# Optimization experiments

Hardware: AMD Instinct MI355X
Metric: run time of the kernel (lower is better)

Reference implementation:

```python
import jax, jax.numpy as jnp
from jax import lax
import numpy as np

I, H = 2048, 128
EPS = 1e-5


def setup_inputs() -> dict:
    key = jax.random.key(0)
    ks = jax.random.split(key, 12)
    s_ih = 1.0 / np.sqrt(H)  # torch nn.RNN init: U(-1/sqrt(H), 1/sqrt(H))
    s_fc = 1.0 / np.sqrt(H)
    u = lambda k, shape, s: jax.random.uniform(k, shape, jnp.float32, -s, s)
    return {
        "x": jax.random.normal(ks[0], (64, 512, I), jnp.float32),
        "W_ih": u(ks[1], (H, I), s_ih),
        "b_ih": u(ks[2], (H,), s_ih),
        "W_hh": u(ks[3], (H, H), s_ih),
        "b_hh": u(ks[4], (H,), s_ih),
        "W1": u(ks[5], (H, H), s_fc),
        "b1": u(ks[6], (H,), s_fc),
        "W2": u(ks[7], (H, H), s_fc),
        "b2": u(ks[8], (H,), s_fc),
        "gamma": jnp.ones((H,), jnp.float32),
        "beta": jnp.zeros((H,), jnp.float32),
    }


def reference(x, W_ih, b_ih, W_hh, b_hh, W1, b1, W2, b2, gamma, beta):
    B = x.shape[0]
    # Precompute input projection for all timesteps: [B, T, H]
    xp = jnp.einsum('bti,hi->bth', x, W_ih) + b_ih

    def step(h, xt):  # h: [B, H], xt: [B, H]
        h_new = jnp.tanh(xt + h @ W_hh.T + b_hh)
        return h_new, None

    h0 = jnp.zeros((B, H), x.dtype)
    hT, _ = lax.scan(step, h0, jnp.swapaxes(xp, 0, 1))  # scan over T

    z = jax.nn.relu(hT @ W1.T + b1)
    z = jax.nn.relu(z @ W2.T + b2)
    mu = jnp.mean(z, axis=-1, keepdims=True)
    var = jnp.mean(jnp.square(z - mu), axis=-1, keepdims=True)
    return gamma * (z - mu) * lax.rsqrt(var + EPS) + beta
```

## Files before the change

### kernel.cpp

```cpp
#include <hip/hip_runtime.h>


typedef __bf16 bf16x8 __attribute__((ext_vector_type(8)));
typedef float  f32x4  __attribute__((ext_vector_type(4)));

#define T_STEPS 512
#define I_DIM   2048
#define H_DIM   128
#define B_DIM   64
#define M_TOT   (B_DIM * T_STEPS)

__device__ __forceinline__ unsigned short f2bf(float f) {
    unsigned int u = __float_as_uint(f);
    u += 0x7FFFu + ((u >> 16) & 1u);
    return (unsigned short)(u >> 16);
}

#define BM  128
#define BK  64
#define LDK 72

__global__ __launch_bounds__(256) void gemm_xp(
    const float* __restrict__ x,
    const float* __restrict__ w,
    const float* __restrict__ b_ih,
    const float* __restrict__ b_hh,
    float* __restrict__ xp)
{
    __shared__ __align__(16) unsigned short As[BM * LDK];
    __shared__ __align__(16) unsigned short Bs[H_DIM * LDK];

    const int tid = threadIdx.x;
    const int m0  = blockIdx.x * BM;

    const int r0 = tid >> 4;
    const int c4 = tid & 15;

    const int lane = tid & 63;
    const int wave = tid >> 6;
    const int wm   = (wave >> 1) * 64;
    const int wn   = (wave & 1) * 64;
    const int l16  = lane & 15;
    const int quad = lane >> 4;

    f32x4 acc[4][4] = {};

    float4 ar[8], br[8];

    auto load_tiles = [&](int k0) {
        #pragma unroll
        for (int i = 0; i < 8; ++i)
            ar[i] = *(const float4*)(x + (size_t)(m0 + i * 16 + r0) * I_DIM + k0 + c4 * 4);
        #pragma unroll
        for (int i = 0; i < 8; ++i)
            br[i] = *(const float4*)(w + (size_t)(i * 16 + r0) * I_DIM + k0 + c4 * 4);
    };

    auto store_tiles = [&]() {
        #pragma unroll
        for (int i = 0; i < 8; ++i) {
            ushort4 v;
            v.x = f2bf(ar[i].x); v.y = f2bf(ar[i].y);
            v.z = f2bf(ar[i].z); v.w = f2bf(ar[i].w);
            *(ushort4*)(As + (i * 16 + r0) * LDK + c4 * 4) = v;
        }
        #pragma unroll
        for (int i = 0; i < 8; ++i) {
            ushort4 v;
            v.x = f2bf(br[i].x); v.y = f2bf(br[i].y);
            v.z = f2bf(br[i].z); v.w = f2bf(br[i].w);
            *(ushort4*)(Bs + (i * 16 + r0) * LDK + c4 * 4) = v;
        }
    };

    load_tiles(0);

    for (int k0 = 0; k0 < I_DIM; k0 += BK) {
        __syncthreads();
        store_tiles();
        if (k0 + BK < I_DIM) load_tiles(k0 + BK);
        __syncthreads();

        #pragma unroll
        for (int kt = 0; kt < 2; ++kt) {
            bf16x8 af[4], bfr[4];
            #pragma unroll
            for (int i = 0; i < 4; ++i)
                af[i] = *(const bf16x8*)(As + (wm + i * 16 + l16) * LDK + kt * 32 + quad * 8);
            #pragma unroll
            for (int i = 0; i < 4; ++i)
                bfr[i] = *(const bf16x8*)(Bs + (wn + i * 16 + l16) * LDK + kt * 32 + quad * 8);
            #pragma unroll
            for (int i = 0; i < 4; ++i)
                #pragma unroll
                for (int j = 0; j < 4; ++j)
                    acc[i][j] = __builtin_amdgcn_mfma_f32_16x16x32_bf16(af[i], bfr[j], acc[i][j], 0, 0, 0);
        }
    }

    #pragma unroll
    for (int j = 0; j < 4; ++j) {
        const int col  = wn + j * 16 + l16;
        const float bias = b_ih[col] + b_hh[col];
        #pragma unroll
        for (int i = 0; i < 4; ++i) {
            #pragma unroll
            for (int r = 0; r < 4; ++r) {
                const int row = wm + i * 16 + quad * 4 + r;
                xp[(size_t)(m0 + row) * H_DIM + col] = acc[i][j][r] + bias;
            }
        }
    }
}

__global__ __launch_bounds__(256) void rnn_tail(
    const float* __restrict__ xp,
    const float* __restrict__ Whh,
    const float* __restrict__ W1, const float* __restrict__ b1,
    const float* __restrict__ W2, const float* __restrict__ b2,
    const float* __restrict__ gamma, const float* __restrict__ beta,
    float* __restrict__ out)
{
    __shared__ float hs[2][H_DIM];
    __shared__ float zb[H_DIM];
    __shared__ float red[4][2];

    const int tid  = threadIdx.x;
    const int b    = blockIdx.x;
    const int j    = tid >> 1;
    const int half = tid & 1;

    float4 wr[16];
    {
        const float4* wrow = (const float4*)(Whh + j * H_DIM + half * 64);
        #pragma unroll
        for (int i = 0; i < 16; ++i) wr[i] = wrow[i];
    }

    if (tid < H_DIM) hs[0][tid] = 0.f;
    const float* xpp = xp + (size_t)b * T_STEPS * H_DIM;
    float xv = xpp[j];
    __syncthreads();

    for (int t = 0; t < T_STEPS; ++t) {
        float xnext = (t < T_STEPS - 1) ? xpp[(t + 1) * H_DIM + j] : 0.f;

        const float4* hv = (const float4*)(hs[t & 1] + half * 64);
        float p0 = 0.f, p1 = 0.f, p2 = 0.f, p3 = 0.f;
        #pragma unroll
        for (int i = 0; i < 16; i += 4) {
            float4 h0 = hv[i], h1 = hv[i + 1], h2 = hv[i + 2], h3 = hv[i + 3];
            p0 += wr[i].x     * h0.x + wr[i].y     * h0.y + wr[i].z     * h0.z + wr[i].w     * h0.w;
            p1 += wr[i + 1].x * h1.x + wr[i + 1].y * h1.y + wr[i + 1].z * h1.z + wr[i + 1].w * h1.w;
            p2 += wr[i + 2].x * h2.x + wr[i + 2].y * h2.y + wr[i + 2].z * h2.z + wr[i + 2].w * h2.w;
            p3 += wr[i + 3].x * h3.x + wr[i + 3].y * h3.y + wr[i + 3].z * h3.z + wr[i + 3].w * h3.w;
        }
        float p = (p0 + p1) + (p2 + p3);
        p += __shfl_xor(p, 1);

        float a  = xv + p;
        float e  = __expf(-2.f * fabsf(a));
        float th = (1.f - e) / (1.f + e);
        th = copysignf(th, a);

        if (half == 0) hs[(t + 1) & 1][j] = th;
        xv = xnext;
        __syncthreads();
    }

    {
        const float4* wv = (const float4*)(W1 + j * H_DIM + half * 64);
        const float4* hv = (const float4*)(hs[0] + half * 64);
        float p0 = 0.f, p1 = 0.f;
        #pragma unroll
        for (int i = 0; i < 16; i += 2) {
            float4 w0 = wv[i], w1_ = wv[i + 1], h0 = hv[i], h1 = hv[i + 1];
            p0 += w0.x * h0.x + w0.y * h0.y + w0.z * h0.z + w0.w * h0.w;
            p1 += w1_.x * h1.x + w1_.y * h1.y + w1_.z * h1.z + w1_.w * h1.w;
        }
        float p = p0 + p1;
        p += __shfl_xor(p, 1);
        float z = fmaxf(p + b1[j], 0.f);
        if (half == 0) zb[j] = z;
    }
    __syncthreads();

    {
        const float4* wv = (const float4*)(W2 + j * H_DIM + half * 64);
        const float4* zv = (const float4*)(zb + half * 64);
        float p0 = 0.f, p1 = 0.f;
        #pragma unroll
        for (int i = 0; i < 16; i += 2) {
            float4 w0 = wv[i], w1_ = wv[i + 1], z0 = zv[i], z1 = zv[i + 1];
            p0 += w0.x * z0.x + w0.y * z0.y + w0.z * z0.z + w0.w * z0.w;
            p1 += w1_.x * z1.x + w1_.y * z1.y + w1_.z * z1.z + w1_.w * z1.w;
        }
        float p = p0 + p1;
        p += __shfl_xor(p, 1);
        float z2 = fmaxf(p + b2[j], 0.f);
        if (half == 0) hs[1][j] = z2;
    }
    __syncthreads();

    float v = (tid < H_DIM) ? hs[1][tid] : 0.f;
    float s = v, q = v * v;
    #pragma unroll
    for (int o = 1; o < 64; o <<= 1) {
        s += __shfl_xor(s, o);
        q += __shfl_xor(q, o);
    }
    const int lane = tid & 63, wave = tid >> 6;
    if (lane == 0) { red[wave][0] = s; red[wave][1] = q; }
    __syncthreads();
    float S = red[0][0] + red[1][0] + red[2][0] + red[3][0];
    float Q = red[0][1] + red[1][1] + red[2][1] + red[3][1];
    float mu   = S * (1.f / 128.f);
    float var  = Q * (1.f / 128.f) - mu * mu;
    float rstd = rsqrtf(var + 1e-5f);
    if (tid < H_DIM)
        out[b * H_DIM + tid] = gamma[tid] * (v - mu) * rstd + beta[tid];
}

extern "C" void kernel_launch(void* const* d_in, const int* in_sizes, int n_in,
                              void* d_out, int out_size, void* d_ws, size_t ws_size,
                              hipStream_t stream) {
    const float* x     = (const float*)d_in[0];
    const float* W_ih  = (const float*)d_in[1];
    const float* b_ih  = (const float*)d_in[2];
    const float* W_hh  = (const float*)d_in[3];
    const float* b_hh  = (const float*)d_in[4];
    const float* W1    = (const float*)d_in[5];
    const float* b1    = (const float*)d_in[6];
    const float* W2    = (const float*)d_in[7];
    const float* b2    = (const float*)d_in[8];
    const float* gamma = (const float*)d_in[9];
    const float* beta  = (const float*)d_in[10];
    float* out = (float*)d_out;

    float* xp = (float*)d_ws;

    gemm_xp<<<dim3(M_TOT / BM), dim3(256), 0, stream>>>(x, W_ih, b_ih, b_hh, xp);
    rnn_tail<<<dim3(B_DIM), dim3(256), 0, stream>>>(xp, W_hh, W1, b1, W2, b2,
                                                    gamma, beta, out);
}
```

Measured before the change: 656.0 us.

## Split recurrent matvec across four lanes per row with 512 threads and padded LDS

The recurrent scan kernel now uses 512 threads, so each output row of W_hh is computed by four lanes holding 32 weights each instead of two lanes holding 64. This halves the serial dot-product length per step on the latency-bound recurrence. The hidden state in LDS is padded into chunks to reduce bank conflicts. The per-step __syncthreads is replaced by an explicit lgkmcnt wait plus s_barrier. The cost is an extra shuffle-reduce stage per step and a barrier across more waves.

```diff
diff --git a/kernel.cpp b/kernel.cpp
--- a/kernel.cpp
+++ b/kernel.cpp
@@ -113,7 +113,9 @@
     }
 }
 
-__global__ __launch_bounds__(256) void rnn_tail(
+#define CH_PAD 36
+
+__global__ __launch_bounds__(512) void rnn_tail(
     const float* __restrict__ xp,
     const float* __restrict__ Whh,
     const float* __restrict__ W1, const float* __restrict__ b1,
@@ -121,23 +123,23 @@
     const float* __restrict__ gamma, const float* __restrict__ beta,
     float* __restrict__ out)
 {
-    __shared__ float hs[2][H_DIM];
-    __shared__ float zb[H_DIM];
-    __shared__ float red[4][2];
-
-    const int tid  = threadIdx.x;
-    const int b    = blockIdx.x;
-    const int j    = tid >> 1;
-    const int half = tid & 1;
-
-    float4 wr[16];
+    __shared__ float hs[2][4][CH_PAD];
+    __shared__ float zb[4][CH_PAD];
+    __shared__ float red[8][2];
+
+    const int tid = threadIdx.x;
+    const int b   = blockIdx.x;
+    const int j   = tid >> 2;
+    const int q   = tid & 3;
+
+    float4 wr[8];
     {
-        const float4* wrow = (const float4*)(Whh + j * H_DIM + half * 64);
-        #pragma unroll
-        for (int i = 0; i < 16; ++i) wr[i] = wrow[i];
-    }
-
-    if (tid < H_DIM) hs[0][tid] = 0.f;
+        const float4* wrow = (const float4*)(Whh + j * H_DIM + q * 32);
+        #pragma unroll
+        for (int i = 0; i < 8; ++i) wr[i] = wrow[i];
+    }
+
+    if (tid < H_DIM) hs[0][tid >> 5][tid & 31] = 0.f;
     const float* xpp = xp + (size_t)b * T_STEPS * H_DIM;
     float xv = xpp[j];
     __syncthreads();
@@ -145,10 +147,10 @@
     for (int t = 0; t < T_STEPS; ++t) {
         float xnext = (t < T_STEPS - 1) ? xpp[(t + 1) * H_DIM + j] : 0.f;
 
-        const float4* hv = (const float4*)(hs[t & 1] + half * 64);
+        const float4* hv = (const float4*)(hs[t & 1][q]);
         float p0 = 0.f, p1 = 0.f, p2 = 0.f, p3 = 0.f;
         #pragma unroll
-        for (int i = 0; i < 16; i += 4) {
+        for (int i = 0; i < 8; i += 4) {
             float4 h0 = hv[i], h1 = hv[i + 1], h2 = hv[i + 2], h3 = hv[i + 3];
             p0 += wr[i].x     * h0.x + wr[i].y     * h0.y + wr[i].z     * h0.z + wr[i].w     * h0.w;
             p1 += wr[i + 1].x * h1.x + wr[i + 1].y * h1.y + wr[i + 1].z * h1.z + wr[i + 1].w * h1.w;
@@ -157,63 +159,69 @@
         }
         float p = (p0 + p1) + (p2 + p3);
         p += __shfl_xor(p, 1);
+        p += __shfl_xor(p, 2);
 
         float a  = xv + p;
         float e  = __expf(-2.f * fabsf(a));
         float th = (1.f - e) / (1.f + e);
         th = copysignf(th, a);
 
-        if (half == 0) hs[(t + 1) & 1][j] = th;
+        if (q == 0) hs[(t + 1) & 1][j >> 5][j & 31] = th;
         xv = xnext;
-        __syncthreads();
+        asm volatile("s_waitcnt lgkmcnt(0)" ::: "memory");
+        __builtin_amdgcn_s_barrier();
+        asm volatile("" ::: "memory");
     }
 
     {
-        const float4* wv = (const float4*)(W1 + j * H_DIM + half * 64);
-        const float4* hv = (const float4*)(hs[0] + half * 64);
+        const float4* wv = (const float4*)(W1 + j * H_DIM + q * 32);
+        const float4* hv = (const float4*)(hs[0][q]);
         float p0 = 0.f, p1 = 0.f;
         #pragma unroll
-        for (int i = 0; i < 16; i += 2) {
+        for (int i = 0; i < 8; i += 2) {
             float4 w0 = wv[i], w1_ = wv[i + 1], h0 = hv[i], h1 = hv[i + 1];
             p0 += w0.x * h0.x + w0.y * h0.y + w0.z * h0.z + w0.w * h0.w;
             p1 += w1_.x * h1.x + w1_.y * h1.y + w1_.z * h1.z + w1_.w * h1.w;
         }
         float p = p0 + p1;
         p += __shfl_xor(p, 1);
+        p += __shfl_xor(p, 2);
         float z = fmaxf(p + b1[j], 0.f);
-        if (half == 0) zb[j] = z;
+        if (q == 0) zb[j >> 5][j & 31] = z;
     }
     __syncthreads();
 
     {
-        const float4* wv = (const float4*)(W2 + j * H_DIM + half * 64);
-        const float4* zv = (const float4*)(zb + half * 64);
+        const float4* wv = (const float4*)(W2 + j * H_DIM + q * 32);
+        const float4* zv = (const float4*)(zb[q]);
         float p0 = 0.f, p1 = 0.f;
         #pragma unroll
-        for (int i = 0; i < 16; i += 2) {
+        for (int i = 0; i < 8; i += 2) {
             float4 w0 = wv[i], w1_ = wv[i + 1], z0 = zv[i], z1 = zv[i + 1];
             p0 += w0.x * z0.x + w0.y * z0.y + w0.z * z0.z + w0.w * z0.w;
             p1 += w1_.x * z1.x + w1_.y * z1.y + w1_.z * z1.z + w1_.w * z1.w;
         }
         float p = p0 + p1;
         p += __shfl_xor(p, 1);
+        p += __shfl_xor(p, 2);
         float z2 = fmaxf(p + b2[j], 0.f);
-        if (half == 0) hs[1][j] = z2;
-    }
-    __syncthreads();
-
-    float v = (tid < H_DIM) ? hs[1][tid] : 0.f;
-    float s = v, q = v * v;
+        if (q == 0) hs[1][j >> 5][j & 31] = z2;
+    }
+    __syncthreads();
+
+    float v = (tid < H_DIM) ? hs[1][tid >> 5][tid & 31] : 0.f;
+    float s = v, sq = v * v;
     #pragma unroll
     for (int o = 1; o < 64; o <<= 1) {
-        s += __shfl_xor(s, o);
-        q += __shfl_xor(q, o);
+        s  += __shfl_xor(s, o);
+        sq += __shfl_xor(sq, o);
     }
     const int lane = tid & 63, wave = tid >> 6;
-    if (lane == 0) { red[wave][0] = s; red[wave][1] = q; }
-    __syncthreads();
-    float S = red[0][0] + red[1][0] + red[2][0] + red[3][0];
-    float Q = red[0][1] + red[1][1] + red[2][1] + red[3][1];
+    if (lane == 0) { red[wave][0] = s; red[wave][1] = sq; }
+    __syncthreads();
+    float S = 0.f, Q = 0.f;
+    #pragma unroll
+    for (int wv2 = 0; wv2 < 8; ++wv2) { S += red[wv2][0]; Q += red[wv2][1]; }
     float mu   = S * (1.f / 128.f);
     float var  = Q * (1.f / 128.f) - mu * mu;
     float rstd = rsqrtf(var + 1e-5f);
@@ -240,6 +248,6 @@
     float* xp = (float*)d_ws;
 
     gemm_xp<<<dim3(M_TOT / BM), dim3(256), 0, stream>>>(x, W_ih, b_ih, b_hh, xp);
-    rnn_tail<<<dim3(B_DIM), dim3(256), 0, stream>>>(xp, W_hh, W1, b1, W2, b2,
+    rnn_tail<<<dim3(B_DIM), dim3(512), 0, stream>>>(xp, W_hh, W1, b1, W2, b2,
                                                     gamma, beta, out);
 }
```

Result: faster. 615.2 us (-6.2%).
